# Kernel optimization log

Measured on AMD Instinct MI355X. Metric: run time of the kernel, lower is better.

## Reference

```python
import jax, jax.numpy as jnp
import numpy as np

NUM_NODES = 100000
EMBED_DIM = 128
NUM_RELATIONS = 64
BATCH = 512


def setup_inputs() -> dict:
    key = jax.random.key(0)
    k1, k2, k3, k4, k5 = jax.random.split(key, 5)
    u = jax.random.randint(k1, (BATCH,), 0, NUM_NODES)
    v = jax.random.randint(k2, (BATCH,), 0, NUM_NODES)
    r = jax.random.randint(k3, (BATCH,), 0, NUM_RELATIONS)
    node_embeddings = jax.random.normal(k4, (NUM_NODES, EMBED_DIM), dtype=jnp.float32)
    relation_matrices = jax.random.normal(k5, (NUM_RELATIONS, EMBED_DIM, EMBED_DIM), dtype=jnp.float32)
    return {"u": u, "v": v, "r": r,
            "node_embeddings": node_embeddings,
            "relation_matrices": relation_matrices}


def reference(u, v, r, node_embeddings, relation_matrices):
    u_embed = node_embeddings[u]            # [B, D]
    v_embed = node_embeddings[v]            # [B, D]
    rel = relation_matrices[r]              # [B, D, D] per-sample gathered matrices
    # torch.matmul([B,D], [B,D,D]) broadcasts u_embed over the relation batch -> [B_rel, B_u, D]
    score = jnp.einsum('ud,bde->bue', u_embed, rel)   # [B, B, D]
    # matmul with v_embed.T [D, B] -> [B, B, B]
    score = jnp.einsum('bue,ve->buv', score, v_embed)  # [B, B, B]
    return jax.nn.sigmoid(score)
```

## Files before the change

### kernel.cpp

```cpp
#include <hip/hip_runtime.h>


#define BATCH 512
#define DIM   128
#define NRELS 64
#define NTHR  256

typedef float floatx4 __attribute__((ext_vector_type(4)));

#define T_ELEMS   ((size_t)NRELS * DIM * BATCH)
#define CNT_OFF   (T_ELEMS)
#define LIST_OFF  (T_ELEMS + 64)
#define WS_NEED   ((T_ELEMS + 64 + (size_t)NRELS * BATCH) * 4)

__global__ __launch_bounds__(NTHR, 2)
void rad_prep_kernel(const int* __restrict__ u_idx,
                     const int* __restrict__ r_idx,
                     const float* __restrict__ nodes,
                     const float* __restrict__ rels,
                     float* __restrict__ ws)
{
    const int bid = (int)blockIdx.x;
    const int t   = (int)threadIdx.x;

    if (bid == NRELS * 8) {
        __shared__ int s_cnt[NRELS];
        int* counts = (int*)(ws + CNT_OFF);
        int* lists  = (int*)(ws + LIST_OFF);
        if (t < NRELS) s_cnt[t] = 0;
        __syncthreads();
        for (int i = t; i < BATCH; i += NTHR) {
            const int rel = r_idx[i];
            const int pos = atomicAdd(&s_cnt[rel], 1);
            lists[rel * BATCH + pos] = i;
        }
        __syncthreads();
        if (t < NRELS) counts[t] = s_cnt[t];
        return;
    }

    const int rel = bid >> 3;
    const int ut0 = (bid & 7) * 64;

    __shared__ __align__(16) float UEsT[DIM * 64];
    __shared__ __align__(16) float Rs[16 * DIM];

    const int tu = t >> 4;
    const int tx = t & 15;

    for (int i = t; i < 64 * (DIM / 4); i += NTHR) {
        const int row = i & 63;
        const int dc  = i >> 6;
        const float4 val = *reinterpret_cast<const float4*>(
            nodes + (size_t)u_idx[ut0 + row] * DIM + dc * 4);
        UEsT[(dc * 4 + 0) * 64 + row] = val.x;
        UEsT[(dc * 4 + 1) * 64 + row] = val.y;
        UEsT[(dc * 4 + 2) * 64 + row] = val.z;
        UEsT[(dc * 4 + 3) * 64 + row] = val.w;
    }

    float accA[4][8];
    #pragma unroll
    for (int i = 0; i < 4; ++i)
        #pragma unroll
        for (int j = 0; j < 8; ++j) accA[i][j] = 0.f;

    const float* Rbase = rels + (size_t)rel * DIM * DIM;
    for (int dch = 0; dch < DIM / 16; ++dch) {
        __syncthreads();
        for (int i = t; i < 16 * (DIM / 4); i += NTHR) {
            const int rr = i >> 5;
            const int cc = i & 31;
            *reinterpret_cast<float4*>(Rs + rr * DIM + cc * 4) =
                *reinterpret_cast<const float4*>(
                    Rbase + (size_t)(dch * 16 + rr) * DIM + cc * 4);
        }
        __syncthreads();
        #pragma unroll
        for (int dd = 0; dd < 16; ++dd) {
            const int d = dch * 16 + dd;
            const float4 a  = *reinterpret_cast<const float4*>(UEsT + d * 64 + tu * 4);
            const float4 b0 = *reinterpret_cast<const float4*>(Rs + dd * DIM + tx * 4);
            const float4 b1 = *reinterpret_cast<const float4*>(Rs + dd * DIM + 64 + tx * 4);
            const float av[4] = {a.x, a.y, a.z, a.w};
            const float bv[8] = {b0.x, b0.y, b0.z, b0.w, b1.x, b1.y, b1.z, b1.w};
            #pragma unroll
            for (int i = 0; i < 4; ++i)
                #pragma unroll
                for (int j = 0; j < 8; ++j)
                    accA[i][j] = fmaf(av[i], bv[j], accA[i][j]);
        }
    }

    #pragma unroll
    for (int j = 0; j < 8; ++j) {
        const int e = (j < 4) ? (tx * 4 + j) : (64 + tx * 4 + (j - 4));
        float4 w4 = make_float4(accA[0][j], accA[1][j], accA[2][j], accA[3][j]);
        *reinterpret_cast<float4*>(
            ws + ((size_t)rel * DIM + e) * BATCH + ut0 + tu * 4) = w4;
    }
}

__global__ __launch_bounds__(NTHR, 2)
void rad_tile_kernel(const int* __restrict__ v_idx,
                     const float* __restrict__ nodes,
                     const float* __restrict__ ws,
                     float* __restrict__ out)
{
    const int bid = (int)blockIdx.x;
    const int x   = bid & 7;
    const int k   = bid >> 3;
    const int rel = k >> 3;
    const int vt0 = (k & 7) * 64;
    const int ut0 = ((x - rel) & 7) * 64;

    const int* counts = (const int*)(ws + CNT_OFF);
    const int* lists  = (const int*)(ws + LIST_OFF) + rel * BATCH;
    const int  mc     = counts[rel];
    if (mc == 0) return;

    __shared__ __align__(16) float TsT[DIM * 64];
    __shared__ __align__(16) float VEsT[DIM * 64];

    const int t  = (int)threadIdx.x;
    const int tu = t >> 4;
    const int tx = t & 15;

    const float* Tbase = ws + (size_t)rel * DIM * BATCH + ut0;
    for (int i = t; i < DIM * 16; i += NTHR) {
        const int e  = i >> 4;
        const int uc = i & 15;
        *reinterpret_cast<float4*>(TsT + e * 64 + uc * 4) =
            *reinterpret_cast<const float4*>(Tbase + (size_t)e * BATCH + uc * 4);
    }
    for (int i = t; i < 64 * (DIM / 4); i += NTHR) {
        const int row = i & 63;
        const int ec  = i >> 6;
        const float4 val = *reinterpret_cast<const float4*>(
            nodes + (size_t)v_idx[vt0 + row] * DIM + ec * 4);
        VEsT[(ec * 4 + 0) * 64 + row] = val.x;
        VEsT[(ec * 4 + 1) * 64 + row] = val.y;
        VEsT[(ec * 4 + 2) * 64 + row] = val.z;
        VEsT[(ec * 4 + 3) * 64 + row] = val.w;
    }
    __syncthreads();

    float acc[4][4];
    #pragma unroll
    for (int i = 0; i < 4; ++i)
        #pragma unroll
        for (int j = 0; j < 4; ++j) acc[i][j] = 0.f;

    #pragma unroll 8
    for (int e = 0; e < DIM; ++e) {
        const float4 a = *reinterpret_cast<const float4*>(TsT  + e * 64 + tu * 4);
        const float4 b = *reinterpret_cast<const float4*>(VEsT + e * 64 + tx * 4);
        const float av[4] = {a.x, a.y, a.z, a.w};
        const float bv[4] = {b.x, b.y, b.z, b.w};
        #pragma unroll
        for (int i = 0; i < 4; ++i)
            #pragma unroll
            for (int j = 0; j < 4; ++j)
                acc[i][j] = fmaf(av[i], bv[j], acc[i][j]);
    }

    floatx4 sg[4];
    #pragma unroll
    for (int i = 0; i < 4; ++i) {
        sg[i].x = 1.f / (1.f + __expf(-acc[i][0]));
        sg[i].y = 1.f / (1.f + __expf(-acc[i][1]));
        sg[i].z = 1.f / (1.f + __expf(-acc[i][2]));
        sg[i].w = 1.f / (1.f + __expf(-acc[i][3]));
    }

    for (int m = 0; m < mc; ++m) {
        const int bb = lists[m];
        float* obase = out + (size_t)bb * BATCH * BATCH + vt0 + tx * 4;
        #pragma unroll
        for (int i = 0; i < 4; ++i) {
            __builtin_nontemporal_store(
                sg[i], reinterpret_cast<floatx4*>(
                           obase + (size_t)(ut0 + tu * 4 + i) * BATCH));
        }
    }
}

__device__ __forceinline__ void lds_barrier() {
    asm volatile("s_waitcnt lgkmcnt(0)" ::: "memory");
    __builtin_amdgcn_s_barrier();
    __builtin_amdgcn_sched_barrier(0);
}

__global__ __launch_bounds__(NTHR, 2)
void rad_fused_kernel(const int* __restrict__ u_idx,
                      const int* __restrict__ v_idx,
                      const int* __restrict__ r_idx,
                      const float* __restrict__ nodes,
                      const float* __restrict__ rels,
                      float* __restrict__ out)
{
    const int bid = (int)blockIdx.x;
    const int rel = ((bid & 7) << 3) | (bid >> 6);
    const int ut0 = ((bid >> 3) & 7) * 64;

    __shared__ int s_match[BATCH];
    __shared__ int s_mc;
    __shared__ __align__(16) float s_TsT[DIM * 64];
    __shared__ __align__(16) float s_buf[DIM * 64 + 16 * DIM];

    const int t  = (int)threadIdx.x;
    const int tu = t >> 4;
    const int tx = t & 15;

    if (t == 0) s_mc = 0;
    __syncthreads();
    for (int i = t; i < BATCH; i += NTHR) {
        if (r_idx[i] == rel) {
            int p = atomicAdd(&s_mc, 1);
            s_match[p] = i;
        }
    }

    float* UEsT = s_buf;
    float* Rs   = s_buf + DIM * 64;

    for (int i = t; i < 64 * (DIM / 4); i += NTHR) {
        const int row = i & 63;
        const int dc  = i >> 6;
        const float4 val = *reinterpret_cast<const float4*>(
            nodes + (size_t)u_idx[ut0 + row] * DIM + dc * 4);
        UEsT[(dc * 4 + 0) * 64 + row] = val.x;
        UEsT[(dc * 4 + 1) * 64 + row] = val.y;
        UEsT[(dc * 4 + 2) * 64 + row] = val.z;
        UEsT[(dc * 4 + 3) * 64 + row] = val.w;
    }
    __syncthreads();
    const int mc = s_mc;
    if (mc == 0) return;

    float accA[4][8];
    #pragma unroll
    for (int i = 0; i < 4; ++i)
        #pragma unroll
        for (int j = 0; j < 8; ++j) accA[i][j] = 0.f;

    const float* Rbase = rels + (size_t)rel * DIM * DIM;
    for (int dch = 0; dch < DIM / 16; ++dch) {
        for (int i = t; i < 16 * (DIM / 4); i += NTHR) {
            const int rr = i >> 5;
            const int cc = i & 31;
            *reinterpret_cast<float4*>(Rs + rr * DIM + cc * 4) =
                *reinterpret_cast<const float4*>(
                    Rbase + (size_t)(dch * 16 + rr) * DIM + cc * 4);
        }
        lds_barrier();
        #pragma unroll
        for (int dd = 0; dd < 16; ++dd) {
            const int d = dch * 16 + dd;
            const float4 a  = *reinterpret_cast<const float4*>(UEsT + d * 64 + tu * 4);
            const float4 b0 = *reinterpret_cast<const float4*>(Rs + dd * DIM + tx * 4);
            const float4 b1 = *reinterpret_cast<const float4*>(Rs + dd * DIM + 64 + tx * 4);
            const float av[4] = {a.x, a.y, a.z, a.w};
            const float bv[8] = {b0.x, b0.y, b0.z, b0.w, b1.x, b1.y, b1.z, b1.w};
            #pragma unroll
            for (int i = 0; i < 4; ++i)
                #pragma unroll
                for (int j = 0; j < 8; ++j)
                    accA[i][j] = fmaf(av[i], bv[j], accA[i][j]);
        }
        lds_barrier();
    }

    #pragma unroll
    for (int j = 0; j < 8; ++j) {
        const int e = (j < 4) ? (tx * 4 + j) : (64 + tx * 4 + (j - 4));
        #pragma unroll
        for (int i = 0; i < 4; ++i)
            s_TsT[e * 64 + tu * 4 + i] = accA[i][j];
    }

    float* VEsT = s_buf;
    for (int vt = 0; vt < BATCH / 64; ++vt) {
        lds_barrier();
        for (int i = t; i < 64 * (DIM / 4); i += NTHR) {
            const int row = i & 63;
            const int ec  = i >> 6;
            const float4 val = *reinterpret_cast<const float4*>(
                nodes + (size_t)v_idx[vt * 64 + row] * DIM + ec * 4);
            VEsT[(ec * 4 + 0) * 64 + row] = val.x;
            VEsT[(ec * 4 + 1) * 64 + row] = val.y;
            VEsT[(ec * 4 + 2) * 64 + row] = val.z;
            VEsT[(ec * 4 + 3) * 64 + row] = val.w;
        }
        lds_barrier();

        float acc[4][4];
        #pragma unroll
        for (int i = 0; i < 4; ++i)
            #pragma unroll
            for (int j = 0; j < 4; ++j) acc[i][j] = 0.f;

        #pragma unroll 8
        for (int e = 0; e < DIM; ++e) {
            const float4 a = *reinterpret_cast<const float4*>(s_TsT + e * 64 + tu * 4);
            const float4 b = *reinterpret_cast<const float4*>(VEsT  + e * 64 + tx * 4);
            const float av[4] = {a.x, a.y, a.z, a.w};
            const float bv[4] = {b.x, b.y, b.z, b.w};
            #pragma unroll
            for (int i = 0; i < 4; ++i)
                #pragma unroll
                for (int j = 0; j < 4; ++j)
                    acc[i][j] = fmaf(av[i], bv[j], acc[i][j]);
        }

        floatx4 sg[4];
        #pragma unroll
        for (int i = 0; i < 4; ++i) {
            sg[i].x = 1.f / (1.f + __expf(-acc[i][0]));
            sg[i].y = 1.f / (1.f + __expf(-acc[i][1]));
            sg[i].z = 1.f / (1.f + __expf(-acc[i][2]));
            sg[i].w = 1.f / (1.f + __expf(-acc[i][3]));
        }

        for (int m = 0; m < mc; ++m) {
            const int bb = s_match[m];
            float* obase = out + (size_t)bb * BATCH * BATCH + vt * 64 + tx * 4;
            #pragma unroll
            for (int i = 0; i < 4; ++i) {
                __builtin_nontemporal_store(
                    sg[i], reinterpret_cast<floatx4*>(
                               obase + (size_t)(ut0 + tu * 4 + i) * BATCH));
            }
        }
    }
}

extern "C" void kernel_launch(void* const* d_in, const int* in_sizes, int n_in,
                              void* d_out, int out_size, void* d_ws, size_t ws_size,
                              hipStream_t stream) {
    const int*   u_idx = (const int*)d_in[0];
    const int*   v_idx = (const int*)d_in[1];
    const int*   r_idx = (const int*)d_in[2];
    const float* nodes = (const float*)d_in[3];
    const float* rels  = (const float*)d_in[4];
    float* out = (float*)d_out;

    if (ws_size >= WS_NEED) {
        float* ws = (float*)d_ws;
        rad_prep_kernel<<<dim3(NRELS * 8 + 1), dim3(NTHR), 0, stream>>>(
            u_idx, r_idx, nodes, rels, ws);
        rad_tile_kernel<<<dim3(NRELS * 8 * 8), dim3(NTHR), 0, stream>>>(
            v_idx, nodes, ws, out);
    } else {
        rad_fused_kernel<<<dim3(NRELS * 8), dim3(NTHR), 0, stream>>>(
            u_idx, v_idx, r_idx, nodes, rels, out);
    }
}
```

Measured before the change: 149.3 us.

## Precompute transposed V embeddings in prep kernel; drop LDS staging in tile kernel

The prep kernel gains 8 extra blocks that gather the v embeddings and write them transposed into the workspace. The tile kernel then reads T and V columns straight from global memory (L2-cached) instead of staging them through shared memory, which removes its LDS use and barrier. That allows a higher occupancy target (launch bounds of 6). The cost is repeated global loads per thread in the inner loop, and the kernel's runtime is likely dominated by the large output stores anyway.

Result: slower. 175.9 us (+17.8%).

```diff
diff --git a/kernel.cpp b/kernel.cpp
--- a/kernel.cpp
+++ b/kernel.cpp
@@ -9,12 +9,14 @@
 typedef float floatx4 __attribute__((ext_vector_type(4)));
 
 #define T_ELEMS   ((size_t)NRELS * DIM * BATCH)
-#define CNT_OFF   (T_ELEMS)
-#define LIST_OFF  (T_ELEMS + 64)
-#define WS_NEED   ((T_ELEMS + 64 + (size_t)NRELS * BATCH) * 4)
+#define VET_OFF   (T_ELEMS)
+#define CNT_OFF   (T_ELEMS + (size_t)DIM * BATCH)
+#define LIST_OFF  (CNT_OFF + 64)
+#define WS_NEED   ((LIST_OFF + (size_t)NRELS * BATCH) * 4)
 
 __global__ __launch_bounds__(NTHR, 2)
 void rad_prep_kernel(const int* __restrict__ u_idx,
+                     const int* __restrict__ v_idx,
                      const int* __restrict__ r_idx,
                      const float* __restrict__ nodes,
                      const float* __restrict__ rels,
@@ -38,6 +40,21 @@
         if (t < NRELS) counts[t] = s_cnt[t];
         return;
     }
+    if (bid > NRELS * 8) {
+        const int v0 = (bid - NRELS * 8 - 1) * 64;
+        float* VEt = ws + VET_OFF;
+        for (int i = t; i < 64 * (DIM / 4); i += NTHR) {
+            const int row = i & 63;
+            const int dc  = i >> 6;
+            const float4 val = *reinterpret_cast<const float4*>(
+                nodes + (size_t)v_idx[v0 + row] * DIM + dc * 4);
+            VEt[(dc * 4 + 0) * BATCH + v0 + row] = val.x;
+            VEt[(dc * 4 + 1) * BATCH + v0 + row] = val.y;
+            VEt[(dc * 4 + 2) * BATCH + v0 + row] = val.z;
+            VEt[(dc * 4 + 3) * BATCH + v0 + row] = val.w;
+        }
+        return;
+    }
 
     const int rel = bid >> 3;
     const int ut0 = (bid & 7) * 64;
@@ -101,10 +118,8 @@
     }
 }
 
-__global__ __launch_bounds__(NTHR, 2)
-void rad_tile_kernel(const int* __restrict__ v_idx,
-                     const float* __restrict__ nodes,
-                     const float* __restrict__ ws,
+__global__ __launch_bounds__(NTHR, 6)
+void rad_tile_kernel(const float* __restrict__ ws,
                      float* __restrict__ out)
 {
     const int bid = (int)blockIdx.x;
@@ -119,31 +134,12 @@
     const int  mc     = counts[rel];
     if (mc == 0) return;
 
-    __shared__ __align__(16) float TsT[DIM * 64];
-    __shared__ __align__(16) float VEsT[DIM * 64];
-
     const int t  = (int)threadIdx.x;
     const int tu = t >> 4;
     const int tx = t & 15;
 
-    const float* Tbase = ws + (size_t)rel * DIM * BATCH + ut0;
-    for (int i = t; i < DIM * 16; i += NTHR) {
-        const int e  = i >> 4;
-        const int uc = i & 15;
-        *reinterpret_cast<float4*>(TsT + e * 64 + uc * 4) =
-            *reinterpret_cast<const float4*>(Tbase + (size_t)e * BATCH + uc * 4);
-    }
-    for (int i = t; i < 64 * (DIM / 4); i += NTHR) {
-        const int row = i & 63;
-        const int ec  = i >> 6;
-        const float4 val = *reinterpret_cast<const float4*>(
-            nodes + (size_t)v_idx[vt0 + row] * DIM + ec * 4);
-        VEsT[(ec * 4 + 0) * 64 + row] = val.x;
-        VEsT[(ec * 4 + 1) * 64 + row] = val.y;
-        VEsT[(ec * 4 + 2) * 64 + row] = val.z;
-        VEsT[(ec * 4 + 3) * 64 + row] = val.w;
-    }
-    __syncthreads();
+    const float* Tcol = ws + (size_t)rel * DIM * BATCH + ut0 + tu * 4;
+    const float* Vcol = ws + VET_OFF + vt0 + tx * 4;
 
     float acc[4][4];
     #pragma unroll
@@ -151,17 +147,17 @@
         #pragma unroll
         for (int j = 0; j < 4; ++j) acc[i][j] = 0.f;
 
-    #pragma unroll 8
+    #pragma unroll 4
     for (int e = 0; e < DIM; ++e) {
-        const float4 a = *reinterpret_cast<const float4*>(TsT  + e * 64 + tu * 4);
-        const float4 b = *reinterpret_cast<const float4*>(VEsT + e * 64 + tx * 4);
-        const float av[4] = {a.x, a.y, a.z, a.w};
-        const float bv[4] = {b.x, b.y, b.z, b.w};
+        const float4 tq = *reinterpret_cast<const float4*>(Tcol + (size_t)e * BATCH);
+        const float4 vq = *reinterpret_cast<const float4*>(Vcol + (size_t)e * BATCH);
+        const float tr[4] = {tq.x, tq.y, tq.z, tq.w};
+        const float vc[4] = {vq.x, vq.y, vq.z, vq.w};
         #pragma unroll
         for (int i = 0; i < 4; ++i)
             #pragma unroll
             for (int j = 0; j < 4; ++j)
-                acc[i][j] = fmaf(av[i], bv[j], acc[i][j]);
+                acc[i][j] = fmaf(tr[i], vc[j], acc[i][j]);
     }
 
     floatx4 sg[4];
@@ -175,12 +171,12 @@
 
     for (int m = 0; m < mc; ++m) {
         const int bb = lists[m];
-        float* obase = out + (size_t)bb * BATCH * BATCH + vt0 + tx * 4;
+        float* obase = out + ((size_t)bb << 18) + vt0 + tx * 4;
         #pragma unroll
         for (int i = 0; i < 4; ++i) {
             __builtin_nontemporal_store(
                 sg[i], reinterpret_cast<floatx4*>(
-                           obase + (size_t)(ut0 + tu * 4 + i) * BATCH));
+                           obase + ((size_t)(ut0 + tu * 4 + i) << 9)));
         }
     }
 }
@@ -347,10 +343,10 @@
 
     if (ws_size >= WS_NEED) {
         float* ws = (float*)d_ws;
-        rad_prep_kernel<<<dim3(NRELS * 8 + 1), dim3(NTHR), 0, stream>>>(
-            u_idx, r_idx, nodes, rels, ws);
+        rad_prep_kernel<<<dim3(NRELS * 8 + 1 + 8), dim3(NTHR), 0, stream>>>(
+            u_idx, v_idx, r_idx, nodes, rels, ws);
         rad_tile_kernel<<<dim3(NRELS * 8 * 8), dim3(NTHR), 0, stream>>>(
-            v_idx, nodes, ws, out);
+            ws, out);
     } else {
         rad_fused_kernel<<<dim3(NRELS * 8), dim3(NTHR), 0, stream>>>(
             u_idx, v_idx, r_idx, nodes, rels, out);
```
